# Kernel tuning notes

Hardware: AMD Instinct MI355X
Metric: run time of the kernel (lower is better)

## Reference

```python
import jax, jax.numpy as jnp
import numpy as np

N_NODES = 100000
N_EDGES = 3200000
IN_CH = 256


def setup_inputs() -> dict:
    key = jax.random.key(0)
    ks = jax.random.split(key, 8)
    x = jax.random.normal(ks[0], (N_NODES, IN_CH), dtype=jnp.float32)
    edge_index = jax.random.randint(ks[1], (2, N_EDGES), 0, N_NODES, dtype=jnp.int64)
    alpha = jnp.ones((), dtype=jnp.float32)
    beta = jnp.ones((), dtype=jnp.float32)
    s = 1.0 / np.sqrt(IN_CH)
    W_mlp = jax.random.normal(ks[2], (1, IN_CH), dtype=jnp.float32) * s
    W_lin = jax.random.normal(ks[3], (1, IN_CH), dtype=jnp.float32) * s
    W_gcn = jax.random.normal(ks[4], (1, IN_CH), dtype=jnp.float32) * s
    W_att = jax.random.normal(ks[5], (3, 3), dtype=jnp.float32) * (1.0 / np.sqrt(3))
    b_att = jax.random.normal(ks[6], (3,), dtype=jnp.float32) * 0.1
    return {"x": x, "edge_index": edge_index, "alpha": alpha, "beta": beta,
            "W_mlp": W_mlp, "W_lin": W_lin, "W_gcn": W_gcn,
            "W_att": W_att, "b_att": b_att}


def _gcn_conv(x, edge_index, W_gcn, num_nodes):
    # PyG GCNConv: add self-loops, symmetric normalization, no bias.
    loop = jnp.arange(num_nodes, dtype=edge_index.dtype)
    row = jnp.concatenate([edge_index[0], loop])  # source
    col = jnp.concatenate([edge_index[1], loop])  # target
    deg = jax.ops.segment_sum(jnp.ones_like(col, dtype=x.dtype), col,
                              num_segments=num_nodes)
    dinv = jnp.where(deg > 0, jax.lax.rsqrt(deg), 0.0)
    norm = dinv[row] * dinv[col]                  # [E+N]
    xw = x @ W_gcn.T                               # [N, 1]
    msg = norm[:, None] * xw[row]                  # [E+N, 1]
    return jax.ops.segment_sum(msg, col, num_segments=num_nodes)  # [N, 1]


def reference(x, edge_index, alpha, beta, W_mlp, W_lin, W_gcn, W_att, b_att):
    num_nodes = x.shape[0]
    # score1: in-degree based
    deg = jax.ops.segment_sum(jnp.ones((edge_index.shape[1],), dtype=x.dtype),
                              edge_index[1], num_segments=num_nodes)
    score1 = jax.nn.sigmoid(alpha * jnp.sqrt(deg) + beta)           # [N]
    # score2: tiny MLP
    score2 = jax.nn.sigmoid((x @ W_mlp.T)[:, 0])                    # [N]
    # score3: GCNConv + linear
    gcn_out = _gcn_conv(x, edge_index, W_gcn, num_nodes)            # [N,1]
    score3 = jax.nn.sigmoid((gcn_out + x @ W_lin.T)[:, 0])          # [N]
    scores = jnp.stack([score1, score2, score3], axis=1)            # [N,3]
    weight = jax.nn.softmax(scores @ W_att.T + b_att, axis=1)       # [N,3]
    fitness = jnp.sum(weight * scores, axis=1)                      # [N]
    return fitness
```

## Files before the change

kernel.cpp:

```cpp
#include <hip/hip_runtime.h>
#include <math.h>

#define N_CH    256
#define SBSHIFT 11
#define SBN     2048
#define NSMAX   64
#define CH      4096

__device__ __forceinline__ float sigmoidf_(float v) {
    return 1.0f / (1.0f + expf(-v));
}

__global__ __launch_bounds__(256) void dots_hist_kernel(
    const float* __restrict__ x,
    const float* __restrict__ Wmlp, const float* __restrict__ Wlin,
    const float* __restrict__ Wgcn, const int* __restrict__ dst,
    float* __restrict__ s2dot, float* __restrict__ s3lin, float* __restrict__ xw,
    int* __restrict__ H1, int* __restrict__ sbT,
    int n_nodes, int n_edges, int ns, int nch)
{
    __shared__ int h[NSMAX];
    if ((int)blockIdx.x < nch) {
        int c = blockIdx.x;
        if (threadIdx.x < NSMAX) h[threadIdx.x] = 0;
        __syncthreads();
        int start = c * CH;
        #pragma unroll
        for (int m = 0; m < 4; ++m) {
            int e = start + (m * 256 + (int)threadIdx.x) * 4;
            if (e + 3 < n_edges) {
                int4 d4 = *(const int4*)(dst + e);
                atomicAdd(&h[d4.x >> SBSHIFT], 1);
                atomicAdd(&h[d4.y >> SBSHIFT], 1);
                atomicAdd(&h[d4.z >> SBSHIFT], 1);
                atomicAdd(&h[d4.w >> SBSHIFT], 1);
            } else {
                int eEnd = e + 4; if (eEnd > n_edges) eEnd = n_edges;
                for (int ee = e; ee < eEnd; ++ee)
                    atomicAdd(&h[dst[ee] >> SBSHIFT], 1);
            }
        }
        __syncthreads();
        if (threadIdx.x < NSMAX) {
            int v = (threadIdx.x < (unsigned)ns) ? h[threadIdx.x] : 0;
            H1[(size_t)c * NSMAX + threadIdx.x] = v;
            if (v) atomicAdd(&sbT[threadIdx.x], v);
        }
        return;
    }

    int wave = ((int)blockIdx.x - nch) * 4 + ((int)threadIdx.x >> 6);
    int lane = threadIdx.x & 63;
    int n0 = wave * 8;
    if (n0 >= n_nodes) return;
    float4 wm = ((const float4*)Wmlp)[lane];
    float4 wl = ((const float4*)Wlin)[lane];
    float4 wg = ((const float4*)Wgcn)[lane];
    int nEnd = n0 + 8; if (nEnd > n_nodes) nEnd = n_nodes;
    for (int node = n0; node < nEnd; ++node) {
        float4 v = ((const float4*)(x + (size_t)node * N_CH))[lane];
        float d0 = v.x*wm.x + v.y*wm.y + v.z*wm.z + v.w*wm.w;
        float d1 = v.x*wl.x + v.y*wl.y + v.z*wl.z + v.w*wl.w;
        float d2 = v.x*wg.x + v.y*wg.y + v.z*wg.z + v.w*wg.w;
        #pragma unroll
        for (int off = 32; off; off >>= 1) {
            d0 += __shfl_down(d0, off, 64);
            d1 += __shfl_down(d1, off, 64);
            d2 += __shfl_down(d2, off, 64);
        }
        if (lane == 0) { s2dot[node] = d0; s3lin[node] = d1; xw[node] = d2; }
    }
}

__global__ __launch_bounds__(64) void seed_kernel(
    const int* __restrict__ sbT, int* __restrict__ sbsG, int* __restrict__ cstG,
    int* __restrict__ cursor, int ns)
{
    __shared__ int sbsL[NSMAX + 1], cstL[NSMAX + 1];
    if (threadIdx.x == 0) {
        int run = 0, c = 0;
        for (int i = 0; i < ns; ++i) {
            sbsL[i] = run; cstL[i] = c;
            int len = sbT[i];
            run += len;
            c += (len + CH - 1) / CH;
        }
        sbsL[ns] = run; cstL[ns] = c;
    }
    __syncthreads();
    int t = threadIdx.x;
    if (t <= ns) { sbsG[t] = sbsL[t]; cstG[t] = cstL[t]; }
    if (t < ns)  cursor[t] = sbsL[t];
}

__global__ __launch_bounds__(256) void scatter_kernel(
    const int* __restrict__ src, const int* __restrict__ dst,
    const int* __restrict__ H1, int* __restrict__ cursor,
    int* __restrict__ cpack, int n_edges, int ns)
{
    __shared__ int lp[NSMAX + 1];
    __shared__ int h[NSMAX];
    __shared__ int pos0[NSMAX];
    __shared__ int sorted[CH];

    int c = blockIdx.x;
    if (threadIdx.x < NSMAX) h[threadIdx.x] = H1[(size_t)c * NSMAX + threadIdx.x];
    __syncthreads();
    if (threadIdx.x == 0) {
        int run = 0;
        for (int i = 0; i < ns; ++i) { lp[i] = run; run += h[i]; }
        lp[ns] = run;
    }
    __syncthreads();
    if (threadIdx.x < (unsigned)ns) {
        int cb = h[threadIdx.x];
        pos0[threadIdx.x] = cb ? atomicAdd(&cursor[threadIdx.x], cb) : 0;
        h[threadIdx.x] = 0;
    }
    __syncthreads();

    int start = c * CH;
    int cnt = n_edges - start; if (cnt > CH) cnt = CH;

    #pragma unroll
    for (int m = 0; m < 4; ++m) {
        int e = start + (m * 256 + (int)threadIdx.x) * 4;
        if (e + 3 < n_edges) {
            int4 s4 = *(const int4*)(src + e);
            int4 d4 = *(const int4*)(dst + e);
            int ss[4] = {s4.x, s4.y, s4.z, s4.w};
            int dd[4] = {d4.x, d4.y, d4.z, d4.w};
            #pragma unroll
            for (int j = 0; j < 4; ++j) {
                int d = dd[j];
                int sb = d >> SBSHIFT;
                int r = atomicAdd(&h[sb], 1);
                sorted[lp[sb] + r] = ss[j] | ((d & (SBN - 1)) << 17);
            }
        } else {
            int eEnd = e + 4; if (eEnd > n_edges) eEnd = n_edges;
            for (int ee = e; ee < eEnd; ++ee) {
                int d = dst[ee];
                int sb = d >> SBSHIFT;
                int r = atomicAdd(&h[sb], 1);
                sorted[lp[sb] + r] = src[ee] | ((d & (SBN - 1)) << 17);
            }
        }
    }
    __syncthreads();
    for (int p = threadIdx.x; p < cnt; p += 256) {
        int lo = 0, hi = ns;
        while (hi - lo > 1) { int mid = (lo + hi) >> 1; if (lp[mid] <= p) lo = mid; else hi = mid; }
        cpack[pos0[lo] + (p - lp[lo])] = sorted[p];
    }
}

__global__ __launch_bounds__(256) void chunkDeg_kernel(
    const int* __restrict__ cpack, const int* __restrict__ sbsG,
    const int* __restrict__ cstG, int* __restrict__ partialD, int ns)
{
    __shared__ int sbsL[NSMAX + 1], cstL[NSMAX + 1];
    __shared__ int cnt[SBN];
    int t = threadIdx.x;
    if (t <= ns) { sbsL[t] = sbsG[t]; cstL[t] = cstG[t]; }
    for (int i = t; i < SBN; i += 256) cnt[i] = 0;
    __syncthreads();
    int c = blockIdx.x;
    if (c >= cstL[ns]) return;
    int lo = 0, hi = ns;
    while (hi - lo > 1) { int mid = (lo + hi) >> 1; if (cstL[mid] <= c) lo = mid; else hi = mid; }
    int sb = lo, i0 = c - cstL[sb];
    int base = sbsL[sb] + i0 * CH;
    int len = sbsL[sb + 1] - base; if (len > CH) len = CH;

    #pragma unroll
    for (int m = 0; m < 4; ++m) {
        int e = (m * 256 + t) * 4;
        if (e + 3 < len) {
            int4 w4 = *(const int4*)(cpack + base + e);
            atomicAdd(&cnt[w4.x >> 17], 1);
            atomicAdd(&cnt[w4.y >> 17], 1);
            atomicAdd(&cnt[w4.z >> 17], 1);
            atomicAdd(&cnt[w4.w >> 17], 1);
        } else {
            int eEnd = e + 4; if (eEnd > len) eEnd = len;
            for (int ee = e; ee < eEnd; ++ee)
                atomicAdd(&cnt[cpack[base + ee] >> 17], 1);
        }
    }
    __syncthreads();
    int* row = partialD + (size_t)c * SBN;
    for (int i = t; i < SBN; i += 256) row[i] = cnt[i];
}

__global__ __launch_bounds__(256) void reduceDeg_kernel(
    const int* __restrict__ partialD, const int* __restrict__ cstG,
    const float* __restrict__ xw,
    float* __restrict__ degf, float* __restrict__ dinv, float* __restrict__ sxw,
    int n_nodes)
{
    int i = blockIdx.x * 256 + threadIdx.x;
    if (i >= n_nodes) return;
    int sb = i >> SBSHIFT, li = i & (SBN - 1);
    int c0 = cstG[sb], c1 = cstG[sb + 1];
    int d = 0;
    for (int c = c0; c < c1; ++c) d += partialD[(size_t)c * SBN + li];
    float df = (float)d;
    degf[i] = df;
    float di = rsqrtf(df + 1.0f);
    dinv[i] = di;
    sxw[i]  = di * xw[i];
}

__global__ __launch_bounds__(256) void chunkAcc_kernel(
    const int* __restrict__ cpack, const int* __restrict__ sbsG,
    const int* __restrict__ cstG, const float* __restrict__ sxw,
    float* __restrict__ partialF, int ns)
{
    __shared__ int sbsL[NSMAX + 1], cstL[NSMAX + 1];
    __shared__ float facc[SBN];
    int t = threadIdx.x;
    if (t <= ns) { sbsL[t] = sbsG[t]; cstL[t] = cstG[t]; }
    for (int i = t; i < SBN; i += 256) facc[i] = 0.0f;
    __syncthreads();
    int c = blockIdx.x;
    if (c >= cstL[ns]) return;
    int lo = 0, hi = ns;
    while (hi - lo > 1) { int mid = (lo + hi) >> 1; if (cstL[mid] <= c) lo = mid; else hi = mid; }
    int sb = lo, i0 = c - cstL[sb];
    int base = sbsL[sb] + i0 * CH;
    int len = sbsL[sb + 1] - base; if (len > CH) len = CH;

    #pragma unroll
    for (int m = 0; m < 4; ++m) {
        int e = (m * 256 + t) * 4;
        if (e + 3 < len) {
            int4 w4 = *(const int4*)(cpack + base + e);
            atomicAdd(&facc[w4.x >> 17], sxw[w4.x & 0x1FFFF]);
            atomicAdd(&facc[w4.y >> 17], sxw[w4.y & 0x1FFFF]);
            atomicAdd(&facc[w4.z >> 17], sxw[w4.z & 0x1FFFF]);
            atomicAdd(&facc[w4.w >> 17], sxw[w4.w & 0x1FFFF]);
        } else {
            int eEnd = e + 4; if (eEnd > len) eEnd = len;
            for (int ee = e; ee < eEnd; ++ee) {
                int w = cpack[base + ee];
                atomicAdd(&facc[w >> 17], sxw[w & 0x1FFFF]);
            }
        }
    }
    __syncthreads();
    float* row = partialF + (size_t)c * SBN;
    for (int i = t; i < SBN; i += 256) row[i] = facc[i];
}

__global__ __launch_bounds__(256) void reduceFinal_kernel(
    const float* __restrict__ partialF, const int* __restrict__ cstG,
    const float* __restrict__ degf, const float* __restrict__ dinv,
    const float* __restrict__ xw, const float* __restrict__ s2dot,
    const float* __restrict__ s3lin,
    const float* __restrict__ alpha, const float* __restrict__ beta,
    const float* __restrict__ Watt, const float* __restrict__ batt,
    float* __restrict__ out, int n_nodes)
{
    int i = blockIdx.x * 256 + threadIdx.x;
    if (i >= n_nodes) return;
    int sb = i >> SBSHIFT, li = i & (SBN - 1);
    int c0 = cstG[sb], c1 = cstG[sb + 1];
    float acc = 0.0f;
    for (int c = c0; c < c1; ++c) acc += partialF[(size_t)c * SBN + li];

    float dn = dinv[i];
    float g  = acc * dn + dn * dn * xw[i];
    float s1 = sigmoidf_(alpha[0] * sqrtf(degf[i]) + beta[0]);
    float s2 = sigmoidf_(s2dot[i]);
    float s3 = sigmoidf_(g + s3lin[i]);

    float z0 = Watt[0]*s1 + Watt[1]*s2 + Watt[2]*s3 + batt[0];
    float z1 = Watt[3]*s1 + Watt[4]*s2 + Watt[5]*s3 + batt[1];
    float z2 = Watt[6]*s1 + Watt[7]*s2 + Watt[8]*s3 + batt[2];

    float m  = fmaxf(z0, fmaxf(z1, z2));
    float e0 = expf(z0 - m), e1 = expf(z1 - m), e2 = expf(z2 - m);
    float inv = 1.0f / (e0 + e1 + e2);
    out[i] = (e0 * s1 + e1 * s2 + e2 * s3) * inv;
}

extern "C" void kernel_launch(void* const* d_in, const int* in_sizes, int n_in,
                              void* d_out, int out_size, void* d_ws, size_t ws_size,
                              hipStream_t stream) {
    const float* x     = (const float*)d_in[0];
    const int*   ei    = (const int*)d_in[1];
    const float* alpha = (const float*)d_in[2];
    const float* beta  = (const float*)d_in[3];
    const float* Wmlp  = (const float*)d_in[4];
    const float* Wlin  = (const float*)d_in[5];
    const float* Wgcn  = (const float*)d_in[6];
    const float* Watt  = (const float*)d_in[7];
    const float* batt  = (const float*)d_in[8];
    float* out = (float*)d_out;

    int n_nodes = in_sizes[0] / N_CH;
    int n_edges = in_sizes[1] / 2;
    const int* src = ei;
    const int* dst = ei + n_edges;

    int ns  = (n_nodes + SBN - 1) >> SBSHIFT;
    int nch = (n_edges + CH - 1) / CH;
    int maxChunks = nch + ns;

    size_t off = 0;
    int*   cpack    = (int*)d_ws;          off += (((size_t)n_edges + 1023) & ~(size_t)1023);
    int*   H1       = (int*)d_ws + off;    off += (((size_t)nch * NSMAX + 1023) & ~(size_t)1023);
    int*   sbT      = (int*)d_ws + off;    off += 128;
    int*   sbsG     = (int*)d_ws + off;    off += 128;
    int*   cstG     = (int*)d_ws + off;    off += 128;
    int*   cursor   = (int*)d_ws + off;    off += 128;
    int*   partialD = (int*)d_ws + off;    off += (size_t)maxChunks * SBN;
    float* partialF = (float*)d_ws + off;  off += (size_t)maxChunks * SBN;
    float* s2dot    = (float*)d_ws + off;  off += (((size_t)n_nodes + 1023) & ~(size_t)1023);
    float* s3lin    = (float*)d_ws + off;  off += (((size_t)n_nodes + 1023) & ~(size_t)1023);
    float* xw       = (float*)d_ws + off;  off += (((size_t)n_nodes + 1023) & ~(size_t)1023);
    float* degf     = (float*)d_ws + off;  off += (((size_t)n_nodes + 1023) & ~(size_t)1023);
    float* dinv     = (float*)d_ws + off;  off += (((size_t)n_nodes + 1023) & ~(size_t)1023);
    float* sxw      = (float*)d_ws + off;  off += (((size_t)n_nodes + 1023) & ~(size_t)1023);

    hipMemsetAsync(sbT, 0, 128 * sizeof(int), stream);

    int dotsBlocks = (n_nodes + 31) / 32;
    dots_hist_kernel<<<nch + dotsBlocks, 256, 0, stream>>>(
        x, Wmlp, Wlin, Wgcn, dst, s2dot, s3lin, xw, H1, sbT,
        n_nodes, n_edges, ns, nch);

    seed_kernel<<<1, 64, 0, stream>>>(sbT, sbsG, cstG, cursor, ns);

    scatter_kernel<<<nch, 256, 0, stream>>>(src, dst, H1, cursor, cpack,
                                            n_edges, ns);

    chunkDeg_kernel<<<maxChunks, 256, 0, stream>>>(cpack, sbsG, cstG, partialD, ns);

    reduceDeg_kernel<<<(n_nodes + 255) / 256, 256, 0, stream>>>(
        partialD, cstG, xw, degf, dinv, sxw, n_nodes);

    chunkAcc_kernel<<<maxChunks, 256, 0, stream>>>(cpack, sbsG, cstG, sxw,
                                                   partialF, ns);

    reduceFinal_kernel<<<(n_nodes + 255) / 256, 256, 0, stream>>>(
        partialF, cstG, degf, dinv, xw, s2dot, s3lin,
        alpha, beta, Watt, batt, out, n_nodes);
}
```

Measured before the change: 264.4 us.

## Drop global histogram atomics and memset; reduce bucket totals in seed kernel

Histogram blocks now write per-chunk bucket counts in a transposed [bucket][chunk] layout and no longer issue global atomics into a totals array. The single-block seed kernel sums each bucket's row with wave reductions instead, which also removes the hipMemsetAsync launch. Separately, the dot-product path now assigns one node per wave rather than eight, launching many more blocks to raise memory-level parallelism. The cost is a serial single-block reduction over about 50 x 782 entries and more block scheduling overhead for the dot products.

```diff
diff --git a/kernel.cpp b/kernel.cpp
--- a/kernel.cpp
+++ b/kernel.cpp
@@ -16,7 +16,7 @@
     const float* __restrict__ Wmlp, const float* __restrict__ Wlin,
     const float* __restrict__ Wgcn, const int* __restrict__ dst,
     float* __restrict__ s2dot, float* __restrict__ s3lin, float* __restrict__ xw,
-    int* __restrict__ H1, int* __restrict__ sbT,
+    int* __restrict__ H1,
     int n_nodes, int n_edges, int ns, int nch)
 {
     __shared__ int h[NSMAX];
@@ -41,47 +41,55 @@
             }
         }
         __syncthreads();
-        if (threadIdx.x < NSMAX) {
-            int v = (threadIdx.x < (unsigned)ns) ? h[threadIdx.x] : 0;
-            H1[(size_t)c * NSMAX + threadIdx.x] = v;
-            if (v) atomicAdd(&sbT[threadIdx.x], v);
-        }
+        if (threadIdx.x < (unsigned)ns)
+            H1[(size_t)threadIdx.x * nch + c] = h[threadIdx.x];
         return;
     }
 
-    int wave = ((int)blockIdx.x - nch) * 4 + ((int)threadIdx.x >> 6);
+    int wid  = ((int)blockIdx.x - nch) * 4 + ((int)threadIdx.x >> 6);
     int lane = threadIdx.x & 63;
-    int n0 = wave * 8;
-    if (n0 >= n_nodes) return;
+    if (wid >= n_nodes) return;
+
+    const float4* xr = (const float4*)(x + (size_t)wid * N_CH);
+    float4 v  = xr[lane];
     float4 wm = ((const float4*)Wmlp)[lane];
     float4 wl = ((const float4*)Wlin)[lane];
     float4 wg = ((const float4*)Wgcn)[lane];
-    int nEnd = n0 + 8; if (nEnd > n_nodes) nEnd = n_nodes;
-    for (int node = n0; node < nEnd; ++node) {
-        float4 v = ((const float4*)(x + (size_t)node * N_CH))[lane];
-        float d0 = v.x*wm.x + v.y*wm.y + v.z*wm.z + v.w*wm.w;
-        float d1 = v.x*wl.x + v.y*wl.y + v.z*wl.z + v.w*wl.w;
-        float d2 = v.x*wg.x + v.y*wg.y + v.z*wg.z + v.w*wg.w;
+
+    float d0 = v.x*wm.x + v.y*wm.y + v.z*wm.z + v.w*wm.w;
+    float d1 = v.x*wl.x + v.y*wl.y + v.z*wl.z + v.w*wl.w;
+    float d2 = v.x*wg.x + v.y*wg.y + v.z*wg.z + v.w*wg.w;
+
+    #pragma unroll
+    for (int off = 32; off; off >>= 1) {
+        d0 += __shfl_down(d0, off, 64);
+        d1 += __shfl_down(d1, off, 64);
+        d2 += __shfl_down(d2, off, 64);
+    }
+    if (lane == 0) { s2dot[wid] = d0; s3lin[wid] = d1; xw[wid] = d2; }
+}
+
+__global__ __launch_bounds__(256) void seed_kernel(
+    const int* __restrict__ H1, int* __restrict__ sbsG, int* __restrict__ cstG,
+    int* __restrict__ cursor, int ns, int nch)
+{
+    __shared__ int tot[NSMAX];
+    __shared__ int sbsL[NSMAX + 1], cstL[NSMAX + 1];
+    int wave = threadIdx.x >> 6, lane = threadIdx.x & 63;
+    for (int sb = wave; sb < ns; sb += 4) {
+        int s = 0;
+        const int* row = H1 + (size_t)sb * nch;
+        for (int c = lane; c < nch; c += 64) s += row[c];
         #pragma unroll
-        for (int off = 32; off; off >>= 1) {
-            d0 += __shfl_down(d0, off, 64);
-            d1 += __shfl_down(d1, off, 64);
-            d2 += __shfl_down(d2, off, 64);
-        }
-        if (lane == 0) { s2dot[node] = d0; s3lin[node] = d1; xw[node] = d2; }
-    }
-}
-
-__global__ __launch_bounds__(64) void seed_kernel(
-    const int* __restrict__ sbT, int* __restrict__ sbsG, int* __restrict__ cstG,
-    int* __restrict__ cursor, int ns)
-{
-    __shared__ int sbsL[NSMAX + 1], cstL[NSMAX + 1];
+        for (int off = 32; off; off >>= 1) s += __shfl_down(s, off, 64);
+        if (lane == 0) tot[sb] = s;
+    }
+    __syncthreads();
     if (threadIdx.x == 0) {
         int run = 0, c = 0;
         for (int i = 0; i < ns; ++i) {
             sbsL[i] = run; cstL[i] = c;
-            int len = sbT[i];
+            int len = tot[i];
             run += len;
             c += (len + CH - 1) / CH;
         }
@@ -96,7 +104,7 @@
 __global__ __launch_bounds__(256) void scatter_kernel(
     const int* __restrict__ src, const int* __restrict__ dst,
     const int* __restrict__ H1, int* __restrict__ cursor,
-    int* __restrict__ cpack, int n_edges, int ns)
+    int* __restrict__ cpack, int n_edges, int ns, int nch)
 {
     __shared__ int lp[NSMAX + 1];
     __shared__ int h[NSMAX];
@@ -104,7 +112,9 @@
     __shared__ int sorted[CH];
 
     int c = blockIdx.x;
-    if (threadIdx.x < NSMAX) h[threadIdx.x] = H1[(size_t)c * NSMAX + threadIdx.x];
+    if (threadIdx.x < NSMAX)
+        h[threadIdx.x] = (threadIdx.x < (unsigned)ns)
+                       ? H1[(size_t)threadIdx.x * nch + c] : 0;
     __syncthreads();
     if (threadIdx.x == 0) {
         int run = 0;
@@ -310,8 +320,7 @@
 
     size_t off = 0;
     int*   cpack    = (int*)d_ws;          off += (((size_t)n_edges + 1023) & ~(size_t)1023);
-    int*   H1       = (int*)d_ws + off;    off += (((size_t)nch * NSMAX + 1023) & ~(size_t)1023);
-    int*   sbT      = (int*)d_ws + off;    off += 128;
+    int*   H1       = (int*)d_ws + off;    off += (((size_t)ns * nch + 1023) & ~(size_t)1023);
     int*   sbsG     = (int*)d_ws + off;    off += 128;
     int*   cstG     = (int*)d_ws + off;    off += 128;
     int*   cursor   = (int*)d_ws + off;    off += 128;
@@ -324,17 +333,15 @@
     float* dinv     = (float*)d_ws + off;  off += (((size_t)n_nodes + 1023) & ~(size_t)1023);
     float* sxw      = (float*)d_ws + off;  off += (((size_t)n_nodes + 1023) & ~(size_t)1023);
 
-    hipMemsetAsync(sbT, 0, 128 * sizeof(int), stream);
-
-    int dotsBlocks = (n_nodes + 31) / 32;
+    int dotsBlocks = (n_nodes + 3) / 4;
     dots_hist_kernel<<<nch + dotsBlocks, 256, 0, stream>>>(
-        x, Wmlp, Wlin, Wgcn, dst, s2dot, s3lin, xw, H1, sbT,
+        x, Wmlp, Wlin, Wgcn, dst, s2dot, s3lin, xw, H1,
         n_nodes, n_edges, ns, nch);
 
-    seed_kernel<<<1, 64, 0, stream>>>(sbT, sbsG, cstG, cursor, ns);
+    seed_kernel<<<1, 256, 0, stream>>>(H1, sbsG, cstG, cursor, ns, nch);
 
     scatter_kernel<<<nch, 256, 0, stream>>>(src, dst, H1, cursor, cpack,
-                                            n_edges, ns);
+                                            n_edges, ns, nch);
 
     chunkDeg_kernel<<<maxChunks, 256, 0, stream>>>(cpack, sbsG, cstG, partialD, ns);
 
```

After: 276.4 us. 1.05x slower.
